# Kernel optimization log

Hardware: AMD Instinct MI355X
Metric: run time of the kernel (lower is better)

Reference implementation:

```python
import jax, jax.numpy as jnp
import numpy as np

S = 4096      # total packed tokens
DIM = 1280    # hidden dim
H = 16        # num heads
HD = DIM // H # head dim = 80


def setup_inputs() -> dict:
    key = jax.random.key(0)
    ks = jax.random.split(key, 5)
    hidden_states = jax.random.normal(ks[0], (S, DIM), jnp.float32)
    # realistic rotary tables: [S, HD] with duplicated half-frequencies
    inv_freq = 1.0 / (10000.0 ** (np.arange(0, HD // 2, dtype=np.float64) / (HD // 2)))
    ang = np.arange(S, dtype=np.float64)[:, None] * inv_freq[None, :]          # [S, HD/2]
    emb = np.concatenate([ang, ang], axis=-1)                                   # [S, HD]
    cos = jnp.asarray(np.cos(emb), jnp.float32)
    sin = jnp.asarray(np.sin(emb), jnp.float32)
    scale = 1.0 / np.sqrt(DIM)
    qkv_w = jax.random.normal(ks[1], (3 * DIM, DIM), jnp.float32) * scale
    qkv_b = jax.random.normal(ks[2], (3 * DIM,), jnp.float32) * 0.02
    proj_w = jax.random.normal(ks[3], (DIM, DIM), jnp.float32) * scale
    proj_b = jax.random.normal(ks[4], (DIM,), jnp.float32) * 0.02
    # ragged segment boundaries: must start at 0 and end at S
    cu_seqlens = jnp.asarray([0, 300, 900, 1500, 2300, 2900, 3500, 4000, 4096], jnp.int32)
    return {
        "hidden_states": hidden_states,
        "cos": cos,
        "sin": sin,
        "qkv_w": qkv_w,
        "qkv_b": qkv_b,
        "proj_w": proj_w,
        "proj_b": proj_b,
        "cu_seqlens": cu_seqlens,
    }


def _rotate_half(x):
    x1, x2 = jnp.split(x, 2, axis=-1)
    return jnp.concatenate([-x2, x1], axis=-1)


def reference(hidden_states, cos, sin, qkv_w, qkv_b, proj_w, proj_b, cu_seqlens):
    seq_len, dim = hidden_states.shape
    hd = dim // H
    qkv = (hidden_states @ qkv_w.T + qkv_b).reshape(seq_len, 3, H, hd)
    q, k, v = qkv[:, 0], qkv[:, 1], qkv[:, 2]                 # each [S, H, hd]
    # RoPE in float32, broadcast cos/sin over heads
    c = cos[:, None, :].astype(jnp.float32)
    s = sin[:, None, :].astype(jnp.float32)
    qf = q.astype(jnp.float32)
    kf = k.astype(jnp.float32)
    q = (qf * c + _rotate_half(qf) * s).astype(q.dtype)
    k = (kf * c + _rotate_half(kf) * s).astype(k.dtype)
    # block-diagonal additive mask: segment id per token
    pos = jnp.arange(seq_len)
    seg = jnp.searchsorted(cu_seqlens[1:], pos, side='right')  # [S]
    neg = jnp.finfo(jnp.float32).min
    bias = jnp.where(seg[:, None] == seg[None, :], 0.0, neg)   # [S, S]
    attn = jnp.einsum('shd,thd->hst', q, k) / np.sqrt(hd) + bias[None]
    w = jax.nn.softmax(attn.astype(jnp.float32), axis=-1).astype(q.dtype)
    out = jnp.einsum('hst,thd->shd', w, v).reshape(seq_len, dim)
    return out @ proj_w.T + proj_b
```

## Files before the change

### kernel.cpp

```cpp
#include <hip/hip_runtime.h>
#include <hip/hip_bf16.h>
#include <stdint.h>

#define SQ 4096
#define DM 1280
#define NH 16
#define HDIM 80
#define N_QKV 3840

typedef __attribute__((ext_vector_type(8))) short short8;
typedef __attribute__((ext_vector_type(4))) float f32x4;

__device__ __forceinline__ unsigned short f2bf(float f) {
  union { float f; unsigned int u; } v; v.f = f;
  unsigned int r = v.u + 0x7FFFu + ((v.u >> 16) & 1u);
  return (unsigned short)(r >> 16);
}
__device__ __forceinline__ float bf2f(unsigned short u) {
  union { unsigned int u; float f; } v; v.u = ((unsigned int)u) << 16;
  return v.f;
}

__global__ __launch_bounds__(256) void cvt_f32_bf16(const float* __restrict__ in,
                                                    unsigned short* __restrict__ out, int n4) {
  int i = blockIdx.x * blockDim.x + threadIdx.x;
  if (i >= n4) return;
  float4 v = reinterpret_cast<const float4*>(in)[i];
  ushort4 o;
  o.x = f2bf(v.x); o.y = f2bf(v.y); o.z = f2bf(v.z); o.w = f2bf(v.w);
  reinterpret_cast<ushort4*>(out)[i] = o;
}

__device__ __forceinline__ void gload_lds16(const void* g, void* l) {
  __builtin_amdgcn_global_load_lds(
      (const __attribute__((address_space(1))) void*)g,
      (__attribute__((address_space(3))) void*)l, 16, 0, 0);
}

template <int OUT_BF16>
__global__ __launch_bounds__(256) void gemm_bt(const unsigned short* __restrict__ A,
                                               const unsigned short* __restrict__ B,
                                               const float* __restrict__ bias,
                                               void* __restrict__ C, int M, int N, int K) {
  __shared__ __align__(16) unsigned short As[128 * 32];
  __shared__ __align__(16) unsigned short Bs[128 * 32];
  const int tid = threadIdx.x;
  const int wave = tid >> 6, lane = tid & 63;
  const int r15 = lane & 15, kg = lane >> 4;
  const int wr = wave >> 1, wc = wave & 1;
  const int tm = blockIdx.y * 128, tn = blockIdx.x * 128;

  f32x4 acc[4][4];
#pragma unroll
  for (int i = 0; i < 4; ++i)
#pragma unroll
    for (int j = 0; j < 4; ++j) acc[i][j] = {0.f, 0.f, 0.f, 0.f};

  for (int kt = 0; kt < K; kt += 32) {
    __syncthreads();
#pragma unroll
    for (int j = 0; j < 2; ++j) {
      int slot = wave * 64 + lane + j * 256;
      int row = slot >> 2, k8 = (slot & 3) << 3;
      gload_lds16(A + (size_t)(tm + row) * K + kt + k8, &As[(wave * 64 + j * 256) * 8]);
      gload_lds16(B + (size_t)(tn + row) * K + kt + k8, &Bs[(wave * 64 + j * 256) * 8]);
    }
    __syncthreads();
    short8 af[4], bfr[4];
#pragma unroll
    for (int mi = 0; mi < 4; ++mi)
      af[mi] = *reinterpret_cast<const short8*>(&As[(wr * 64 + mi * 16 + r15) * 32 + kg * 8]);
#pragma unroll
    for (int ni = 0; ni < 4; ++ni)
      bfr[ni] = *reinterpret_cast<const short8*>(&Bs[(wc * 64 + ni * 16 + r15) * 32 + kg * 8]);
#pragma unroll
    for (int mi = 0; mi < 4; ++mi)
#pragma unroll
      for (int ni = 0; ni < 4; ++ni)
        acc[mi][ni] = __builtin_amdgcn_mfma_f32_16x16x32_bf16(af[mi], bfr[ni], acc[mi][ni], 0, 0, 0);
  }
#pragma unroll
  for (int mi = 0; mi < 4; ++mi) {
#pragma unroll
    for (int ni = 0; ni < 4; ++ni) {
      int col = tn + wc * 64 + ni * 16 + r15;
      float bv = bias[col];
#pragma unroll
      for (int r = 0; r < 4; ++r) {
        int row = tm + wr * 64 + mi * 16 + kg * 4 + r;
        float v = acc[mi][ni][r] + bv;
        if (OUT_BF16)
          ((unsigned short*)C)[(size_t)row * N + col] = f2bf(v);
        else
          ((float*)C)[(size_t)row * N + col] = v;
      }
    }
  }
}

__global__ __launch_bounds__(256) void rope_v_kernel(unsigned short* __restrict__ qkv,
                                                     const float* __restrict__ cosb,
                                                     const float* __restrict__ sinb,
                                                     unsigned short* __restrict__ Vt) {
  int h = blockIdx.y, s0 = blockIdx.x * 64;
  __shared__ unsigned short vt[64][80];
  for (int e = threadIdx.x; e < 64 * 40; e += 256) {
    int sl = e / 40, dp = e % 40;
    int s = s0 + sl;
    float c = cosb[s * HDIM + dp];
    float sn = sinb[s * HDIM + dp];
    size_t qb = (size_t)s * N_QKV + h * HDIM;
    float q1 = bf2f(qkv[qb + dp]), q2 = bf2f(qkv[qb + dp + 40]);
    qkv[qb + dp] = f2bf(q1 * c - q2 * sn);
    qkv[qb + dp + 40] = f2bf(q2 * c + q1 * sn);
    size_t kb = qb + DM;
    float k1 = bf2f(qkv[kb + dp]), k2 = bf2f(qkv[kb + dp + 40]);
    qkv[kb + dp] = f2bf(k1 * c - k2 * sn);
    qkv[kb + dp + 40] = f2bf(k2 * c + k1 * sn);
    size_t vb = qb + 2 * DM;
    vt[sl][dp] = qkv[vb + dp];
    vt[sl][dp + 40] = qkv[vb + dp + 40];
  }
  __syncthreads();
  for (int e = threadIdx.x; e < HDIM * 64; e += 256) {
    int d = e >> 6, sl = e & 63;
    Vt[((size_t)h * HDIM + d) * SQ + s0 + sl] = vt[sl][d];
  }
}

template <int CTRL>
__device__ __forceinline__ float dpp_f(float x) {
  int xi = __builtin_bit_cast(int, x);
  int r = __builtin_amdgcn_update_dpp(xi, xi, CTRL, 0xf, 0xf, true);
  return __builtin_bit_cast(float, r);
}
__device__ __forceinline__ float rowmax16(float x) {
  x = fmaxf(x, dpp_f<0xB1>(x));
  x = fmaxf(x, dpp_f<0x4E>(x));
  x = fmaxf(x, dpp_f<0x141>(x));
  x = fmaxf(x, dpp_f<0x140>(x));
  return x;
}
__device__ __forceinline__ float rowsum16(float x) {
  x += dpp_f<0xB1>(x);
  x += dpp_f<0x4E>(x);
  x += dpp_f<0x141>(x);
  x += dpp_f<0x140>(x);
  return x;
}

__global__ __launch_bounds__(256, 2) void attn_kernel(const unsigned short* __restrict__ qkv,
                                                      const unsigned short* __restrict__ Vt,
                                                      const int* __restrict__ cu, int nseg,
                                                      unsigned short* __restrict__ attn_out) {
  constexpr int PROW = 68;
  __shared__ __align__(16) unsigned char Kl[2][64 * 256];
  __shared__ __align__(16) unsigned char Vl[2][80 * 128];
  __shared__ __align__(16) unsigned short Pl[4][16 * PROW];
  __shared__ int cus[32];

  const int tid = threadIdx.x;
  const int wave = tid >> 6, lane = tid & 63;
  const int r15 = lane & 15, kg = lane >> 4;
  const int s7 = r15 & 7;
  const short8 z8 = {0, 0, 0, 0, 0, 0, 0, 0};

  const int b = blockIdx.x;
  const int xcd = b & 7, j = b >> 3;
  const int h = xcd * 2 + (j >> 6);
  const int qt = j & 63;

  if (tid <= nseg) cus[tid] = cu[tid];
  __syncthreads();

  auto seg_of = [&](int pos) {
    int s2 = 0;
    for (int i2 = 1; i2 < nseg; ++i2)
      if (pos >= cus[i2]) s2 = i2;
    return s2;
  };

  const int tbase = qt * 64;
  const int wbase = tbase + wave * 16;
  int rs[4], re[4];
#pragma unroll
  for (int r = 0; r < 4; ++r) {
    int sg = seg_of(wbase + kg * 4 + r);
    rs[r] = cus[sg];
    re[r] = cus[sg + 1];
  }
  const int kb0 = cus[seg_of(tbase)] & ~63;
  const int kend = cus[seg_of(tbase + 63) + 1];
  const int nt = (kend - kb0 + 63) >> 6;

  const unsigned short* qp = qkv + (size_t)(wbase + r15) * N_QKV + h * HDIM;
  short8 qf[3];
#pragma unroll
  for (int ds = 0; ds < 3; ++ds) {
    int d0 = ds * 32 + kg * 8;
    qf[ds] = (d0 < HDIM) ? *reinterpret_cast<const short8*>(qp + d0) : z8;
  }

  float m[4] = {-1e30f, -1e30f, -1e30f, -1e30f};
  float l[4] = {0.f, 0.f, 0.f, 0.f};
  f32x4 acc[5];
#pragma unroll
  for (int dg = 0; dg < 5; ++dg) acc[dg] = {0.f, 0.f, 0.f, 0.f};

  const float scale = 0.1118033988749895f;
  const unsigned short* kbase = qkv + DM + (size_t)h * HDIM;
  const unsigned short* vbase = Vt + (size_t)h * HDIM * SQ;
  unsigned short* pw = &Pl[wave][0];
  const int wub = tid & ~63;

  auto issue_stage = [&](int kb, int buf) {
    unsigned char* kd = &Kl[buf][0];
    unsigned char* vd = &Vl[buf][0];
#pragma unroll
    for (int p = 0; p < 4; ++p) {
      int L = p * 256 + tid;
      int row = L >> 4;
      int c = (L & 15) ^ (row & 7);
      int csrc = (c < 10) ? c : 0;
      gload_lds16(kbase + (size_t)(kb + row) * N_QKV + csrc * 8,
                  kd + (p * 256 + wub) * 16);
    }
#pragma unroll
    for (int p = 0; p < 2; ++p) {
      int L = p * 256 + tid;
      int row = L >> 3;
      int c = (L & 7) ^ (row & 7);
      gload_lds16(vbase + (size_t)row * SQ + kb + c * 8,
                  vd + (p * 256 + wub) * 16);
    }
    {
      int L = 512 + (wub >> 1) + (lane & 31);
      int row = L >> 3;
      int c = (L & 7) ^ (row & 7);
      if (lane < 32)
        gload_lds16(vbase + (size_t)row * SQ + kb + c * 8,
                    vd + (512 + (wub >> 1)) * 16);
    }
  };

  issue_stage(kb0, 0);
  int cur = 0;

  for (int t = 0; t < nt; ++t) {
    const int k0 = kb0 + (t << 6);
    if (t + 1 < nt) {
      issue_stage(k0 + 64, cur ^ 1);
      asm volatile("s_waitcnt vmcnt(7)" ::: "memory");
    } else {
      asm volatile("s_waitcnt vmcnt(0)" ::: "memory");
    }
    __builtin_amdgcn_sched_barrier(0);
    __builtin_amdgcn_s_barrier();

    const unsigned char* Kc = &Kl[cur][0];
    const unsigned char* Vc = &Vl[cur][0];

    f32x4 sa[4];
#pragma unroll
    for (int g = 0; g < 4; ++g) sa[g] = {0.f, 0.f, 0.f, 0.f};
#pragma unroll
    for (int g = 0; g < 4; ++g) {
      const unsigned char* kr = Kc + ((g * 16 + r15) << 8);
#pragma unroll
      for (int ds = 0; ds < 3; ++ds) {
        int d0 = ds * 32 + kg * 8;
        short8 kf = (d0 < HDIM)
            ? *reinterpret_cast<const short8*>(kr + (((ds * 4 + kg) ^ s7) << 4))
            : z8;
        sa[g] = __builtin_amdgcn_mfma_f32_16x16x32_bf16(qf[ds], kf, sa[g], 0, 0, 0);
      }
    }

    short8 vf[5][2];
#pragma unroll
    for (int dg = 0; dg < 5; ++dg)
#pragma unroll
      for (int g2 = 0; g2 < 2; ++g2)
        vf[dg][g2] = *reinterpret_cast<const short8*>(
            Vc + ((dg * 16 + r15) << 7) + (((g2 * 4 + kg) ^ s7) << 4));

    float p[4][4], corr[4];
#pragma unroll
    for (int r = 0; r < 4; ++r) {
      float vv[4];
#pragma unroll
      for (int g = 0; g < 4; ++g) {
        int key = k0 + g * 16 + r15;
        vv[g] = (key >= rs[r] && key < re[r]) ? sa[g][r] * scale : -1e30f;
      }
      float mx = fmaxf(fmaxf(vv[0], vv[1]), fmaxf(vv[2], vv[3]));
      mx = rowmax16(mx);
      float mn = fmaxf(m[r], mx);
      float c = __expf(m[r] - mn);
      float sm = 0.f;
#pragma unroll
      for (int g = 0; g < 4; ++g) {
        p[r][g] = __expf(vv[g] - mn);
        sm += p[r][g];
      }
      sm = rowsum16(sm);
      l[r] = l[r] * c + sm;
      m[r] = mn;
      corr[r] = c;
    }
#pragma unroll
    for (int dg = 0; dg < 5; ++dg) {
      f32x4 t2 = acc[dg];
      t2[0] *= corr[0]; t2[1] *= corr[1]; t2[2] *= corr[2]; t2[3] *= corr[3];
      acc[dg] = t2;
    }

#pragma unroll
    for (int r = 0; r < 4; ++r) {
      unsigned short* prow = pw + (kg * 4 + r) * PROW;
#pragma unroll
      for (int g = 0; g < 4; ++g) prow[g * 16 + r15] = f2bf(p[r][g]);
    }
    asm volatile("s_waitcnt lgkmcnt(0)" ::: "memory");
    __builtin_amdgcn_sched_barrier(0);
    const unsigned short* prd = pw + r15 * PROW;
    union { short8 v; uint2 d[2]; } pu[2];
#pragma unroll
    for (int g2 = 0; g2 < 2; ++g2) {
      pu[g2].d[0] = *reinterpret_cast<const uint2*>(prd + g2 * 32 + kg * 8);
      pu[g2].d[1] = *reinterpret_cast<const uint2*>(prd + g2 * 32 + kg * 8 + 4);
    }

    __builtin_amdgcn_s_setprio(1);
#pragma unroll
    for (int dg = 0; dg < 5; ++dg)
#pragma unroll
      for (int g2 = 0; g2 < 2; ++g2)
        acc[dg] = __builtin_amdgcn_mfma_f32_16x16x32_bf16(pu[g2].v, vf[dg][g2], acc[dg], 0, 0, 0);
    __builtin_amdgcn_s_setprio(0);

    __builtin_amdgcn_s_barrier();
    cur ^= 1;
  }

#pragma unroll
  for (int r = 0; r < 4; ++r) {
    int row = wbase + kg * 4 + r;
    float inv = 1.0f / l[r];
#pragma unroll
    for (int dg = 0; dg < 5; ++dg)
      attn_out[(size_t)row * DM + h * HDIM + dg * 16 + r15] = f2bf(acc[dg][r] * inv);
  }
}

extern "C" void kernel_launch(void* const* d_in, const int* in_sizes, int n_in,
                              void* d_out, int out_size, void* d_ws, size_t ws_size,
                              hipStream_t stream) {
  const float* hidden = (const float*)d_in[0];
  const float* cosb = (const float*)d_in[1];
  const float* sinb = (const float*)d_in[2];
  const float* qkv_w = (const float*)d_in[3];
  const float* qkv_b = (const float*)d_in[4];
  const float* proj_w = (const float*)d_in[5];
  const float* proj_b = (const float*)d_in[6];
  const int* cu = (const int*)d_in[7];
  int nseg = in_sizes[7] - 1;
  float* out = (float*)d_out;

  char* ws = (char*)d_ws;
  unsigned short* Ah = (unsigned short*)(ws);
  unsigned short* Wq = (unsigned short*)(ws + 10485760);
  unsigned short* Wp = (unsigned short*)(ws + 10485760 + 9830400);
  unsigned short* qkvB = (unsigned short*)(ws + 23592960);
  unsigned short* Vt = (unsigned short*)(ws + 23592960 + 31457280);
  unsigned short* attn_out = Ah;

  cvt_f32_bf16<<<dim3((1310720 + 255) / 256), dim3(256), 0, stream>>>(hidden, Ah, 1310720);
  cvt_f32_bf16<<<dim3((1228800 + 255) / 256), dim3(256), 0, stream>>>(qkv_w, Wq, 1228800);
  cvt_f32_bf16<<<dim3((409600 + 255) / 256), dim3(256), 0, stream>>>(proj_w, Wp, 409600);
  gemm_bt<1><<<dim3(30, 32), dim3(256), 0, stream>>>(Ah, Wq, qkv_b, qkvB, SQ, N_QKV, DM);
  rope_v_kernel<<<dim3(64, NH), dim3(256), 0, stream>>>(qkvB, cosb, sinb, Vt);
  attn_kernel<<<dim3(1024), dim3(256), 0, stream>>>(qkvB, Vt, cu, nseg, attn_out);
  gemm_bt<0><<<dim3(10, 32), dim3(256), 0, stream>>>(attn_out, Wp, proj_b, out, SQ, DM, DM);
}
```

Before: 211.8 us.

## Triple-buffer GEMM loads, remap blocks for XCD locality, fuse conversion kernels

```diff
diff --git a/kernel.cpp b/kernel.cpp
--- a/kernel.cpp
+++ b/kernel.cpp
@@ -21,10 +21,20 @@
   return v.f;
 }
 
-__global__ __launch_bounds__(256) void cvt_f32_bf16(const float* __restrict__ in,
-                                                    unsigned short* __restrict__ out, int n4) {
-  int i = blockIdx.x * blockDim.x + threadIdx.x;
-  if (i >= n4) return;
+__global__ __launch_bounds__(256) void cvt_all(const float* __restrict__ hidden,
+                                               const float* __restrict__ qkv_w,
+                                               const float* __restrict__ proj_w,
+                                               unsigned short* __restrict__ oh,
+                                               unsigned short* __restrict__ oq,
+                                               unsigned short* __restrict__ op) {
+  int b = blockIdx.x;
+  const float* in;
+  unsigned short* out;
+  int base;
+  if (b < 5120) { in = hidden; out = oh; base = b; }
+  else if (b < 9920) { in = qkv_w; out = oq; base = b - 5120; }
+  else { in = proj_w; out = op; base = b - 9920; }
+  int i = base * 256 + threadIdx.x;
   float4 v = reinterpret_cast<const float4*>(in)[i];
   ushort4 o;
   o.x = f2bf(v.x); o.y = f2bf(v.y); o.z = f2bf(v.z); o.w = f2bf(v.w);
@@ -38,47 +48,85 @@
 }
 
 template <int OUT_BF16>
-__global__ __launch_bounds__(256) void gemm_bt(const unsigned short* __restrict__ A,
-                                               const unsigned short* __restrict__ B,
-                                               const float* __restrict__ bias,
-                                               void* __restrict__ C, int M, int N, int K) {
-  __shared__ __align__(16) unsigned short As[128 * 32];
-  __shared__ __align__(16) unsigned short Bs[128 * 32];
+__global__ __launch_bounds__(256, 3) void gemm_bt(const unsigned short* __restrict__ A,
+                                                  const unsigned short* __restrict__ B,
+                                                  const float* __restrict__ bias,
+                                                  void* __restrict__ C, int M, int N, int K,
+                                                  int nbx) {
+  __shared__ __align__(16) unsigned short As[3][128 * 32];
+  __shared__ __align__(16) unsigned short Bs[3][128 * 32];
   const int tid = threadIdx.x;
   const int wave = tid >> 6, lane = tid & 63;
   const int r15 = lane & 15, kg = lane >> 4;
   const int wr = wave >> 1, wc = wave & 1;
-  const int tm = blockIdx.y * 128, tn = blockIdx.x * 128;
+
+  const int b = blockIdx.x;
+  const int c = b & 7, i = b >> 3;
+  const int by = (c & 3) * 8 + (i & 7);
+  const int bx = (c >> 2) * (nbx >> 1) + (i >> 3);
+  const int tm = by * 128, tn = bx * 128;
 
   f32x4 acc[4][4];
 #pragma unroll
-  for (int i = 0; i < 4; ++i)
-#pragma unroll
-    for (int j = 0; j < 4; ++j) acc[i][j] = {0.f, 0.f, 0.f, 0.f};
-
-  for (int kt = 0; kt < K; kt += 32) {
-    __syncthreads();
-#pragma unroll
-    for (int j = 0; j < 2; ++j) {
-      int slot = wave * 64 + lane + j * 256;
-      int row = slot >> 2, k8 = (slot & 3) << 3;
-      gload_lds16(A + (size_t)(tm + row) * K + kt + k8, &As[(wave * 64 + j * 256) * 8]);
-      gload_lds16(B + (size_t)(tn + row) * K + kt + k8, &Bs[(wave * 64 + j * 256) * 8]);
-    }
-    __syncthreads();
+  for (int x = 0; x < 4; ++x)
+#pragma unroll
+    for (int j = 0; j < 4; ++j) acc[x][j] = {0.f, 0.f, 0.f, 0.f};
+
+  const int slot0 = wave * 64 + lane;
+  const int row0 = slot0 >> 2, k80 = (slot0 & 3) << 3;
+  const int slot1 = slot0 + 256;
+  const int row1 = slot1 >> 2, k81 = (slot1 & 3) << 3;
+  const unsigned short* Arow0 = A + (size_t)(tm + row0) * K + k80;
+  const unsigned short* Arow1 = A + (size_t)(tm + row1) * K + k81;
+  const unsigned short* Brow0 = B + (size_t)(tn + row0) * K + k80;
+  const unsigned short* Brow1 = B + (size_t)(tn + row1) * K + k81;
+  const int ldsoff0 = (wave * 64) * 8;
+  const int ldsoff1 = (wave * 64 + 256) * 8;
+
+  auto stage = [&](int kt, int buf) {
+    gload_lds16(Arow0 + kt, &As[buf][ldsoff0]);
+    gload_lds16(Arow1 + kt, &As[buf][ldsoff1]);
+    gload_lds16(Brow0 + kt, &Bs[buf][ldsoff0]);
+    gload_lds16(Brow1 + kt, &Bs[buf][ldsoff1]);
+  };
+
+  const int nk = K >> 5;
+  stage(0, 0);
+  if (nk > 1) stage(32, 1);
+
+  int buf = 0;
+  for (int t = 0; t < nk; ++t) {
+    if (t + 2 < nk) {
+      stage((t + 2) << 5, (buf + 2) % 3);
+      asm volatile("s_waitcnt vmcnt(8)" ::: "memory");
+    } else if (t + 1 < nk) {
+      asm volatile("s_waitcnt vmcnt(4)" ::: "memory");
+    } else {
+      asm volatile("s_waitcnt vmcnt(0)" ::: "memory");
+    }
+    __builtin_amdgcn_sched_barrier(0);
+    __builtin_amdgcn_s_barrier();
+
     short8 af[4], bfr[4];
 #pragma unroll
     for (int mi = 0; mi < 4; ++mi)
-      af[mi] = *reinterpret_cast<const short8*>(&As[(wr * 64 + mi * 16 + r15) * 32 + kg * 8]);
+      af[mi] = *reinterpret_cast<const short8*>(&As[buf][(wr * 64 + mi * 16 + r15) * 32 + kg * 8]);
 #pragma unroll
     for (int ni = 0; ni < 4; ++ni)
-      bfr[ni] = *reinterpret_cast<const short8*>(&Bs[(wc * 64 + ni * 16 + r15) * 32 + kg * 8]);
+      bfr[ni] = *reinterpret_cast<const short8*>(&Bs[buf][(wc * 64 + ni * 16 + r15) * 32 + kg * 8]);
+    __builtin_amdgcn_s_setprio(1);
 #pragma unroll
     for (int mi = 0; mi < 4; ++mi)
 #pragma unroll
       for (int ni = 0; ni < 4; ++ni)
         acc[mi][ni] = __builtin_amdgcn_mfma_f32_16x16x32_bf16(af[mi], bfr[ni], acc[mi][ni], 0, 0, 0);
-  }
+    __builtin_amdgcn_s_setprio(0);
+
+    __builtin_amdgcn_s_barrier();
+    __builtin_amdgcn_sched_barrier(0);
+    buf = (buf + 1) % 3;
+  }
+
 #pragma unroll
   for (int mi = 0; mi < 4; ++mi) {
 #pragma unroll
@@ -375,11 +423,9 @@
   unsigned short* Vt = (unsigned short*)(ws + 23592960 + 31457280);
   unsigned short* attn_out = Ah;
 
-  cvt_f32_bf16<<<dim3((1310720 + 255) / 256), dim3(256), 0, stream>>>(hidden, Ah, 1310720);
-  cvt_f32_bf16<<<dim3((1228800 + 255) / 256), dim3(256), 0, stream>>>(qkv_w, Wq, 1228800);
-  cvt_f32_bf16<<<dim3((409600 + 255) / 256), dim3(256), 0, stream>>>(proj_w, Wp, 409600);
-  gemm_bt<1><<<dim3(30, 32), dim3(256), 0, stream>>>(Ah, Wq, qkv_b, qkvB, SQ, N_QKV, DM);
+  cvt_all<<<dim3(11520), dim3(256), 0, stream>>>(hidden, qkv_w, proj_w, Ah, Wq, Wp);
+  gemm_bt<1><<<dim3(960), dim3(256), 0, stream>>>(Ah, Wq, qkv_b, qkvB, SQ, N_QKV, DM, 30);
   rope_v_kernel<<<dim3(64, NH), dim3(256), 0, stream>>>(qkvB, cosb, sinb, Vt);
   attn_kernel<<<dim3(1024), dim3(256), 0, stream>>>(qkvB, Vt, cu, nseg, attn_out);
-  gemm_bt<0><<<dim3(10, 32), dim3(256), 0, stream>>>(attn_out, Wp, proj_b, out, SQ, DM, DM);
-}
+  gemm_bt<0><<<dim3(320), dim3(256), 0, stream>>>(attn_out, Wp, proj_b, out, SQ, DM, DM, 10);
+}
```

Result: faster. 193.7 us (median of 2 runs) (-8.6%).
